# Performance work log

Measured on AMD Instinct MI355X. Metric: run time of the kernel, lower is better.

The kernel has to match this reference:

```python
import jax, jax.numpy as jnp
import numpy as np


def setup_inputs() -> dict:
    key = jax.random.key(0)
    k1, k2 = jax.random.split(key)
    B, N, M = 32, 4096, 4096
    pred = jax.random.normal(k1, (B, N, 3), dtype=jnp.float32)
    target = jax.random.normal(k2, (B, M, 3), dtype=jnp.float32)
    return {"pred": pred, "target": target}


def reference(pred, target):
    # pairwise euclidean distances: [B, N, M]
    # d2 = |p|^2 + |t|^2 - 2 p.t  (matches torch.cdist p=2)
    p2 = jnp.sum(pred * pred, axis=-1)                      # [B, N]
    t2 = jnp.sum(target * target, axis=-1)                  # [B, M]
    pt = jnp.einsum('bnd,bmd->bnm', pred, target)           # [B, N, M]
    d2 = p2[:, :, None] + t2[:, None, :] - 2.0 * pt
    dist = jnp.sqrt(jnp.maximum(d2, 0.0))                   # [B, N, M]
    min_d = jnp.min(dist, axis=2)                           # [B, N]
    return jnp.mean(min_d)
```

## Files before the change

### kernel.cpp

```cpp
#include <hip/hip_runtime.h>


typedef short bf16x8 __attribute__((ext_vector_type(8)));
typedef float f32x16 __attribute__((ext_vector_type(16)));

constexpr int Bc = 32;
constexpr int Nc = 4096;
constexpr int Mc = 4096;
constexpr int BLOCK = 256;
constexpr int PTS = Bc * Nc;

__device__ __forceinline__ unsigned short brne(float x) {
  unsigned u = __float_as_uint(x);
  return (unsigned short)((u + 0x7FFFu + ((u >> 16) & 1u)) >> 16);
}
__device__ __forceinline__ float bf2f(unsigned short h) {
  return __uint_as_float(((unsigned)h) << 16);
}
__device__ __forceinline__ unsigned pack(unsigned short lo, unsigned short hi) {
  return (unsigned)lo | ((unsigned)hi << 16);
}

__global__ __launch_bounds__(BLOCK)
__attribute__((amdgpu_waves_per_eu(4, 4)))
void emd_main_kernel(const float* __restrict__ pred,
                     const float* __restrict__ target,
                     float* __restrict__ slices) {
  __shared__ uint4 lds[2048];

  const int b = blockIdx.x >> 5;
  const int pg = (blockIdx.x >> 1) & 15;
  const int th = blockIdx.x & 1;
  const int lane = threadIdx.x & 63;
  const int half = lane >> 5;
  const int l31 = lane & 31;
  const int wave = threadIdx.x >> 6;
  const unsigned short ONE = 0x3F80;

  {
    const size_t i = (size_t)b * Nc + pg * 256 + threadIdx.x;
    float x = pred[3 * i], y = pred[3 * i + 1], z = pred[3 * i + 2];
    unsigned short xh = brne(x), xl = brne(x - bf2f(xh));
    unsigned short yh = brne(y), yl = brne(y - bf2f(yh));
    unsigned short zh = brne(z), zl = brne(z - bf2f(zh));
    float p2 = fmaf(x, x, fmaf(y, y, z * z));
    unsigned short ph = brne(p2), pl = brne(p2 - bf2f(ph));
    lds[threadIdx.x] =
        make_uint4(pack(xh, xh), pack(xl, yh), pack(yh, yl), pack(zh, zh));
    lds[256 + threadIdx.x] =
        make_uint4(pack(zl, ph), pack(pl, ONE), pack(ONE, 0), 0);
  }
  __syncthreads();

  uint4 a0u = lds[half * 256 + wave * 64 + l31];
  uint4 a1u = lds[half * 256 + wave * 64 + 32 + l31];
  bf16x8 a0 = *(const bf16x8*)&a0u;
  bf16x8 a1 = *(const bf16x8*)&a1u;

  f32x16 r0, r1;
#pragma unroll
  for (int i = 0; i < 16; ++i) { r0[i] = 3.4e38f; r1[i] = 3.4e38f; }

  for (int c = 0; c < 2; ++c) {
    __syncthreads();
    const size_t tbase = (size_t)b * Mc + th * 2048 + c * 1024;
    {
      const float4* tp4 = (const float4*)(target + tbase * 3);
      float4 f0 = tp4[3 * threadIdx.x + 0];
      float4 f1 = tp4[3 * threadIdx.x + 1];
      float4 f2 = tp4[3 * threadIdx.x + 2];
      float cx[4] = {f0.x, f0.w, f1.z, f2.y};
      float cy[4] = {f0.y, f1.x, f1.w, f2.z};
      float cz[4] = {f0.z, f1.y, f2.x, f2.w};
#pragma unroll
      for (int j = 0; j < 4; ++j) {
        const int pt = 4 * threadIdx.x + j;
        float x = -2.0f * cx[j], y = -2.0f * cy[j], z = -2.0f * cz[j];
        unsigned short xh = brne(x), xl = brne(x - bf2f(xh));
        unsigned short yh = brne(y), yl = brne(y - bf2f(yh));
        unsigned short zh = brne(z), zl = brne(z - bf2f(zh));
        float t2 = 0.25f * fmaf(x, x, fmaf(y, y, z * z));
        unsigned short t2h = brne(t2), t2l = brne(t2 - bf2f(t2h));
        lds[pt] =
            make_uint4(pack(xh, xl), pack(xh, yh), pack(yl, yh), pack(zh, zl));
        lds[1024 + pt] =
            make_uint4(pack(zh, ONE), pack(ONE, t2h), pack(t2l, 0), 0);
      }
    }
    __syncthreads();

    const int base = half * 1024 + l31;
#pragma unroll 1
    for (int t = 0; t < 32; t += 4) {
      uint4 bu0 = lds[base + (t + 0) * 32];
      uint4 bu1 = lds[base + (t + 1) * 32];
      uint4 bu2 = lds[base + (t + 2) * 32];
      uint4 bu3 = lds[base + (t + 3) * 32];
      bf16x8 bf0 = *(const bf16x8*)&bu0;
      bf16x8 bf1 = *(const bf16x8*)&bu1;
      bf16x8 bf2 = *(const bf16x8*)&bu2;
      bf16x8 bf3 = *(const bf16x8*)&bu3;
      f32x16 z{};
      f32x16 d00 = __builtin_amdgcn_mfma_f32_32x32x16_bf16(a0, bf0, z, 0, 0, 0);
      f32x16 d01 = __builtin_amdgcn_mfma_f32_32x32x16_bf16(a0, bf1, z, 0, 0, 0);
      f32x16 d02 = __builtin_amdgcn_mfma_f32_32x32x16_bf16(a0, bf2, z, 0, 0, 0);
      f32x16 d03 = __builtin_amdgcn_mfma_f32_32x32x16_bf16(a0, bf3, z, 0, 0, 0);
      f32x16 d10 = __builtin_amdgcn_mfma_f32_32x32x16_bf16(a1, bf0, z, 0, 0, 0);
      f32x16 d11 = __builtin_amdgcn_mfma_f32_32x32x16_bf16(a1, bf1, z, 0, 0, 0);
      f32x16 d12 = __builtin_amdgcn_mfma_f32_32x32x16_bf16(a1, bf2, z, 0, 0, 0);
      f32x16 d13 = __builtin_amdgcn_mfma_f32_32x32x16_bf16(a1, bf3, z, 0, 0, 0);
#pragma unroll
      for (int i = 0; i < 16; ++i) {
        r0[i] = fminf(fminf(d00[i], d01[i]), r0[i]);
        r0[i] = fminf(fminf(d02[i], d03[i]), r0[i]);
        r1[i] = fminf(fminf(d10[i], d11[i]), r1[i]);
        r1[i] = fminf(fminf(d12[i], d13[i]), r1[i]);
      }
    }
  }

#pragma unroll
  for (int off = 1; off < 32; off <<= 1) {
#pragma unroll
    for (int i = 0; i < 16; ++i) {
      r0[i] = fminf(r0[i], __shfl_xor(r0[i], off, 64));
      r1[i] = fminf(r1[i], __shfl_xor(r1[i], off, 64));
    }
  }
  if (l31 == 0) {
    float* sl = slices + (size_t)th * PTS + b * Nc + pg * 256 + wave * 64;
#pragma unroll
    for (int i = 0; i < 16; ++i) {
      const int row = (i & 3) + 8 * (i >> 2) + 4 * half;
      sl[row] = fmaxf(r0[i], 0.0f);
      sl[32 + row] = fmaxf(r1[i], 0.0f);
    }
  }
}

__global__ __launch_bounds__(BLOCK) void emd_finish_kernel(
    const float4* __restrict__ slices, float* __restrict__ out) {
  __shared__ float wsum[4];
  const int i = blockIdx.x * BLOCK + threadIdx.x;
  float4 v0 = slices[i];
  float4 v1 = slices[PTS / 4 + i];
  float s = sqrtf(fminf(v0.x, v1.x)) + sqrtf(fminf(v0.y, v1.y)) +
            sqrtf(fminf(v0.z, v1.z)) + sqrtf(fminf(v0.w, v1.w));
#pragma unroll
  for (int off = 32; off > 0; off >>= 1) s += __shfl_down(s, off, 64);
  if ((threadIdx.x & 63) == 0) wsum[threadIdx.x >> 6] = s;
  __syncthreads();
  if (threadIdx.x == 0) {
    float tot = (wsum[0] + wsum[1]) + (wsum[2] + wsum[3]);
    atomicAdd(out, tot * (1.0f / (float)PTS));
  }
}

extern "C" void kernel_launch(void* const* d_in, const int* in_sizes, int n_in,
                              void* d_out, int out_size, void* d_ws, size_t ws_size,
                              hipStream_t stream) {
  const float* pred = (const float*)d_in[0];
  const float* target = (const float*)d_in[1];
  float* out = (float*)d_out;
  float* slices = (float*)d_ws;

  emd_main_kernel<<<dim3(Bc * 16 * 2), dim3(BLOCK), 0, stream>>>(
      pred, target, slices);
  emd_finish_kernel<<<dim3(PTS / 4 / BLOCK), dim3(BLOCK), 0, stream>>>(
      (const float4*)slices, out);
}
```

Before: 81.05 us.

## Swap MFMA operand roles so pred points map to columns, reduce min in registers

Each wave now keeps four pred fragments (128 points) in registers and streams target fragments from LDS as the A operand, so the min over targets lands along the accumulator's row dimension. This lets per-lane min reduction happen in registers, with only one cross-half shuffle instead of a five-step butterfly across 32 lanes. The grid is repartitioned to 512 pred points per block and 4 target slices of 1024, with a single target load phase per block. The finish kernel now combines 4 slices instead of 2, which adds some workspace traffic.

```diff
diff --git a/kernel.cpp b/kernel.cpp
--- a/kernel.cpp
+++ b/kernel.cpp
@@ -9,6 +9,9 @@
 constexpr int Mc = 4096;
 constexpr int BLOCK = 256;
 constexpr int PTS = Bc * Nc;
+constexpr int S = 4;
+constexpr int TPB = 1024;
+constexpr int PPB = 512;
 
 __device__ __forceinline__ unsigned short brne(float x) {
   unsigned u = __float_as_uint(x);
@@ -28,113 +31,97 @@
                      float* __restrict__ slices) {
   __shared__ uint4 lds[2048];
 
-  const int b = blockIdx.x >> 5;
-  const int pg = (blockIdx.x >> 1) & 15;
-  const int th = blockIdx.x & 1;
+  const int pg = blockIdx.x >> 2;
+  const int s = blockIdx.x & 3;
+  const int b = pg >> 3;
   const int lane = threadIdx.x & 63;
   const int half = lane >> 5;
   const int l31 = lane & 31;
   const int wave = threadIdx.x >> 6;
   const unsigned short ONE = 0x3F80;
 
-  {
-    const size_t i = (size_t)b * Nc + pg * 256 + threadIdx.x;
-    float x = pred[3 * i], y = pred[3 * i + 1], z = pred[3 * i + 2];
+#pragma unroll
+  for (int j = 0; j < 2; ++j) {
+    const int p = threadIdx.x + j * BLOCK;
+    const size_t gi = (size_t)pg * PPB + p;
+    float x = pred[3 * gi], y = pred[3 * gi + 1], z = pred[3 * gi + 2];
     unsigned short xh = brne(x), xl = brne(x - bf2f(xh));
     unsigned short yh = brne(y), yl = brne(y - bf2f(yh));
     unsigned short zh = brne(z), zl = brne(z - bf2f(zh));
     float p2 = fmaf(x, x, fmaf(y, y, z * z));
     unsigned short ph = brne(p2), pl = brne(p2 - bf2f(ph));
-    lds[threadIdx.x] =
-        make_uint4(pack(xh, xh), pack(xl, yh), pack(yh, yl), pack(zh, zh));
-    lds[256 + threadIdx.x] =
-        make_uint4(pack(zl, ph), pack(pl, ONE), pack(ONE, 0), 0);
+    lds[p] = make_uint4(pack(xh, xl), pack(xh, yh), pack(yl, yh), pack(zh, zl));
+    lds[512 + p] = make_uint4(pack(zh, ONE), pack(ONE, ph), pack(pl, 0), 0);
   }
   __syncthreads();
 
-  uint4 a0u = lds[half * 256 + wave * 64 + l31];
-  uint4 a1u = lds[half * 256 + wave * 64 + 32 + l31];
-  bf16x8 a0 = *(const bf16x8*)&a0u;
-  bf16x8 a1 = *(const bf16x8*)&a1u;
+  bf16x8 bfr[4];
+#pragma unroll
+  for (int f = 0; f < 4; ++f) {
+    uint4 u = lds[half * 512 + wave * 128 + f * 32 + l31];
+    bfr[f] = *(const bf16x8*)&u;
+  }
+  __syncthreads();
 
-  f32x16 r0, r1;
+  {
+    const size_t tbase = (size_t)b * Mc + s * TPB;
+    const float4* tp4 = (const float4*)(target + tbase * 3);
+    float4 f0 = tp4[3 * threadIdx.x + 0];
+    float4 f1 = tp4[3 * threadIdx.x + 1];
+    float4 f2 = tp4[3 * threadIdx.x + 2];
+    float cx[4] = {f0.x, f0.w, f1.z, f2.y};
+    float cy[4] = {f0.y, f1.x, f1.w, f2.z};
+    float cz[4] = {f0.z, f1.y, f2.x, f2.w};
 #pragma unroll
-  for (int i = 0; i < 16; ++i) { r0[i] = 3.4e38f; r1[i] = 3.4e38f; }
+    for (int j = 0; j < 4; ++j) {
+      const int pt = 4 * threadIdx.x + j;
+      float X = -2.0f * cx[j], Y = -2.0f * cy[j], Z = -2.0f * cz[j];
+      unsigned short Xh = brne(X), Xl = brne(X - bf2f(Xh));
+      unsigned short Yh = brne(Y), Yl = brne(Y - bf2f(Yh));
+      unsigned short Zh = brne(Z), Zl = brne(Z - bf2f(Zh));
+      float t2 = 0.25f * fmaf(X, X, fmaf(Y, Y, Z * Z));
+      unsigned short th = brne(t2), tl = brne(t2 - bf2f(th));
+      lds[pt] =
+          make_uint4(pack(Xh, Xh), pack(Xl, Yh), pack(Yh, Yl), pack(Zh, Zh));
+      lds[1024 + pt] =
+          make_uint4(pack(Zl, th), pack(tl, ONE), pack(ONE, 0), 0);
+    }
+  }
+  __syncthreads();
 
-  for (int c = 0; c < 2; ++c) {
-    __syncthreads();
-    const size_t tbase = (size_t)b * Mc + th * 2048 + c * 1024;
-    {
-      const float4* tp4 = (const float4*)(target + tbase * 3);
-      float4 f0 = tp4[3 * threadIdx.x + 0];
-      float4 f1 = tp4[3 * threadIdx.x + 1];
-      float4 f2 = tp4[3 * threadIdx.x + 2];
-      float cx[4] = {f0.x, f0.w, f1.z, f2.y};
-      float cy[4] = {f0.y, f1.x, f1.w, f2.z};
-      float cz[4] = {f0.z, f1.y, f2.x, f2.w};
+  float rA[4], rB[4];
 #pragma unroll
-      for (int j = 0; j < 4; ++j) {
-        const int pt = 4 * threadIdx.x + j;
-        float x = -2.0f * cx[j], y = -2.0f * cy[j], z = -2.0f * cz[j];
-        unsigned short xh = brne(x), xl = brne(x - bf2f(xh));
-        unsigned short yh = brne(y), yl = brne(y - bf2f(yh));
-        unsigned short zh = brne(z), zl = brne(z - bf2f(zh));
-        float t2 = 0.25f * fmaf(x, x, fmaf(y, y, z * z));
-        unsigned short t2h = brne(t2), t2l = brne(t2 - bf2f(t2h));
-        lds[pt] =
-            make_uint4(pack(xh, xl), pack(xh, yh), pack(yl, yh), pack(zh, zl));
-        lds[1024 + pt] =
-            make_uint4(pack(zh, ONE), pack(ONE, t2h), pack(t2l, 0), 0);
-      }
-    }
-    __syncthreads();
+  for (int f = 0; f < 4; ++f) { rA[f] = 3.4e38f; rB[f] = 3.4e38f; }
 
-    const int base = half * 1024 + l31;
-#pragma unroll 1
-    for (int t = 0; t < 32; t += 4) {
-      uint4 bu0 = lds[base + (t + 0) * 32];
-      uint4 bu1 = lds[base + (t + 1) * 32];
-      uint4 bu2 = lds[base + (t + 2) * 32];
-      uint4 bu3 = lds[base + (t + 3) * 32];
-      bf16x8 bf0 = *(const bf16x8*)&bu0;
-      bf16x8 bf1 = *(const bf16x8*)&bu1;
-      bf16x8 bf2 = *(const bf16x8*)&bu2;
-      bf16x8 bf3 = *(const bf16x8*)&bu3;
-      f32x16 z{};
-      f32x16 d00 = __builtin_amdgcn_mfma_f32_32x32x16_bf16(a0, bf0, z, 0, 0, 0);
-      f32x16 d01 = __builtin_amdgcn_mfma_f32_32x32x16_bf16(a0, bf1, z, 0, 0, 0);
-      f32x16 d02 = __builtin_amdgcn_mfma_f32_32x32x16_bf16(a0, bf2, z, 0, 0, 0);
-      f32x16 d03 = __builtin_amdgcn_mfma_f32_32x32x16_bf16(a0, bf3, z, 0, 0, 0);
-      f32x16 d10 = __builtin_amdgcn_mfma_f32_32x32x16_bf16(a1, bf0, z, 0, 0, 0);
-      f32x16 d11 = __builtin_amdgcn_mfma_f32_32x32x16_bf16(a1, bf1, z, 0, 0, 0);
-      f32x16 d12 = __builtin_amdgcn_mfma_f32_32x32x16_bf16(a1, bf2, z, 0, 0, 0);
-      f32x16 d13 = __builtin_amdgcn_mfma_f32_32x32x16_bf16(a1, bf3, z, 0, 0, 0);
+  const int abase = half * 1024 + l31;
+#pragma unroll 2
+  for (int t = 0; t < 32; ++t) {
+    uint4 au = lds[abase + t * 32];
+    bf16x8 af = *(const bf16x8*)&au;
+    f32x16 z{};
+    f32x16 d0 = __builtin_amdgcn_mfma_f32_32x32x16_bf16(af, bfr[0], z, 0, 0, 0);
+    f32x16 d1 = __builtin_amdgcn_mfma_f32_32x32x16_bf16(af, bfr[1], z, 0, 0, 0);
+    f32x16 d2 = __builtin_amdgcn_mfma_f32_32x32x16_bf16(af, bfr[2], z, 0, 0, 0);
+    f32x16 d3 = __builtin_amdgcn_mfma_f32_32x32x16_bf16(af, bfr[3], z, 0, 0, 0);
 #pragma unroll
-      for (int i = 0; i < 16; ++i) {
-        r0[i] = fminf(fminf(d00[i], d01[i]), r0[i]);
-        r0[i] = fminf(fminf(d02[i], d03[i]), r0[i]);
-        r1[i] = fminf(fminf(d10[i], d11[i]), r1[i]);
-        r1[i] = fminf(fminf(d12[i], d13[i]), r1[i]);
-      }
+    for (int i = 0; i < 16; i += 4) {
+      rA[0] = fminf(fminf(d0[i], d0[i + 1]), rA[0]);
+      rB[0] = fminf(fminf(d0[i + 2], d0[i + 3]), rB[0]);
+      rA[1] = fminf(fminf(d1[i], d1[i + 1]), rA[1]);
+      rB[1] = fminf(fminf(d1[i + 2], d1[i + 3]), rB[1]);
+      rA[2] = fminf(fminf(d2[i], d2[i + 1]), rA[2]);
+      rB[2] = fminf(fminf(d2[i + 2], d2[i + 3]), rB[2]);
+      rA[3] = fminf(fminf(d3[i], d3[i + 1]), rA[3]);
+      rB[3] = fminf(fminf(d3[i + 2], d3[i + 3]), rB[3]);
     }
   }
 
+  const size_t sbase = (size_t)s * PTS + (size_t)pg * PPB + wave * 128;
 #pragma unroll
-  for (int off = 1; off < 32; off <<= 1) {
-#pragma unroll
-    for (int i = 0; i < 16; ++i) {
-      r0[i] = fminf(r0[i], __shfl_xor(r0[i], off, 64));
-      r1[i] = fminf(r1[i], __shfl_xor(r1[i], off, 64));
-    }
-  }
-  if (l31 == 0) {
-    float* sl = slices + (size_t)th * PTS + b * Nc + pg * 256 + wave * 64;
-#pragma unroll
-    for (int i = 0; i < 16; ++i) {
-      const int row = (i & 3) + 8 * (i >> 2) + 4 * half;
-      sl[row] = fmaxf(r0[i], 0.0f);
-      sl[32 + row] = fmaxf(r1[i], 0.0f);
-    }
+  for (int f = 0; f < 4; ++f) {
+    float rr = fminf(rA[f], rB[f]);
+    rr = fminf(rr, __shfl_xor(rr, 32, 64));
+    if (lane < 32) slices[sbase + f * 32 + l31] = fmaxf(rr, 0.0f);
   }
 }
 
@@ -142,13 +129,19 @@
     const float4* __restrict__ slices, float* __restrict__ out) {
   __shared__ float wsum[4];
   const int i = blockIdx.x * BLOCK + threadIdx.x;
-  float4 v0 = slices[i];
-  float4 v1 = slices[PTS / 4 + i];
-  float s = sqrtf(fminf(v0.x, v1.x)) + sqrtf(fminf(v0.y, v1.y)) +
-            sqrtf(fminf(v0.z, v1.z)) + sqrtf(fminf(v0.w, v1.w));
+  float4 m = slices[i];
 #pragma unroll
-  for (int off = 32; off > 0; off >>= 1) s += __shfl_down(s, off, 64);
-  if ((threadIdx.x & 63) == 0) wsum[threadIdx.x >> 6] = s;
+  for (int s = 1; s < S; ++s) {
+    float4 v = slices[(size_t)s * (PTS / 4) + i];
+    m.x = fminf(m.x, v.x);
+    m.y = fminf(m.y, v.y);
+    m.z = fminf(m.z, v.z);
+    m.w = fminf(m.w, v.w);
+  }
+  float ss = sqrtf(m.x) + sqrtf(m.y) + sqrtf(m.z) + sqrtf(m.w);
+#pragma unroll
+  for (int off = 32; off > 0; off >>= 1) ss += __shfl_down(ss, off, 64);
+  if ((threadIdx.x & 63) == 0) wsum[threadIdx.x >> 6] = ss;
   __syncthreads();
   if (threadIdx.x == 0) {
     float tot = (wsum[0] + wsum[1]) + (wsum[2] + wsum[3]);
@@ -164,7 +157,7 @@
   float* out = (float*)d_out;
   float* slices = (float*)d_ws;
 
-  emd_main_kernel<<<dim3(Bc * 16 * 2), dim3(BLOCK), 0, stream>>>(
+  emd_main_kernel<<<dim3((PTS / PPB) * S), dim3(BLOCK), 0, stream>>>(
       pred, target, slices);
   emd_finish_kernel<<<dim3(PTS / 4 / BLOCK), dim3(BLOCK), 0, stream>>>(
       (const float4*)slices, out);
```

New measurement: 75.08 us, median of 2. 1.08x faster.
